# Kernel optimization log

Measured on AMD Instinct MI355X. Metric: run time of the kernel, lower is better.

Reference implementation:

```python
import jax, jax.numpy as jnp
import numpy as np

E, B, D, H, Z = 8, 16384, 512, 512, 64   # experts, batch, input_dim, hidden, latent
NHID = 2                                 # num_mlp_layers - 1 hidden-to-hidden layers


def setup_inputs() -> dict:
    key = jax.random.key(0)
    ks = jax.random.split(key, 12)

    def w(k, shape, fan_in):
        return (jax.random.normal(k, shape, jnp.float32) / np.sqrt(fan_in)).astype(jnp.float32)

    return {
        "x": jax.random.normal(ks[0], (B, D), jnp.float32),
        "eps": jax.random.normal(ks[1], (B, Z), jnp.float32),
        # stacked per-expert parameters (leading axis E)
        "enc_in_w": w(ks[2], (E, D, H), D), "enc_in_b": jnp.zeros((E, H), jnp.float32),
        "enc_hid_w": w(ks[3], (E, NHID, H, H), H), "enc_hid_b": jnp.zeros((E, NHID, H), jnp.float32),
        "mu_w": w(ks[4], (E, H, Z), H), "mu_b": jnp.zeros((E, Z), jnp.float32),
        "lv_w": w(ks[5], (E, H, Z), H), "lv_b": jnp.zeros((E, Z), jnp.float32),
        "dec_in_w": w(ks[6], (E, Z, H), Z), "dec_in_b": jnp.zeros((E, H), jnp.float32),
        "dec_hid_w": w(ks[7], (E, NHID, H, H), H), "dec_hid_b": jnp.zeros((E, NHID, H), jnp.float32),
        "dec_out_w": w(ks[8], (E, H, D), H), "dec_out_b": jnp.zeros((E, D), jnp.float32),
    }


def _moe_forward(x, eps, enc_in_w, enc_in_b, enc_hid_w, enc_hid_b,
                 mu_w, mu_b, lv_w, lv_b,
                 dec_in_w, dec_in_b, dec_hid_w, dec_hid_b, dec_out_w, dec_out_b):
    # ---- every expert tries the problem (dense, all experts over full batch) ----
    h = jax.nn.relu(jnp.einsum('bd,edh->ebh', x, enc_in_w) + enc_in_b[:, None, :])
    for i in range(NHID):
        h = jax.nn.relu(jnp.einsum('ebh,ehk->ebk', h, enc_hid_w[:, i]) + enc_hid_b[:, i, None, :])
    mu = jnp.einsum('ebh,ehz->ebz', h, mu_w) + mu_b[:, None, :]          # [E,B,Z]
    logvar = jnp.einsum('ebh,ehz->ebz', h, lv_w) + lv_b[:, None, :]       # [E,B,Z]
    z = mu + jnp.exp(0.5 * logvar) * eps[None, :, :]                      # reparameterize
    g = jax.nn.relu(jnp.einsum('ebz,ezh->ebh', z, dec_in_w) + dec_in_b[:, None, :])
    for i in range(NHID):
        g = jax.nn.relu(jnp.einsum('ebh,ehk->ebk', g, dec_hid_w[:, i]) + dec_hid_b[:, i, None, :])
    xhat = jnp.einsum('ebh,ehd->ebd', g, dec_out_w) + dec_out_b[:, None, :]  # [E,B,D]

    # ---- per-sample recon loss, pick best expert (torch.min over experts) ----
    recon = jnp.mean((xhat - x[None, :, :]) ** 2, axis=-1)                # [E,B]
    expert_idx = jnp.argmin(recon, axis=0)                                # [B]

    # ---- sparse_others: single fused gather instead of python loop ----
    bi = jnp.arange(x.shape[0])
    return mu[expert_idx, bi], logvar[expert_idx, bi], xhat[expert_idx, bi]


def reference(x, eps, enc_in_w, enc_in_b, enc_hid_w, enc_hid_b,
              mu_w, mu_b, lv_w, lv_b,
              dec_in_w, dec_in_b, dec_hid_w, dec_hid_b, dec_out_w, dec_out_b):
    return _moe_forward(x, eps, enc_in_w, enc_in_b, enc_hid_w, enc_hid_b,
                        mu_w, mu_b, lv_w, lv_b,
                        dec_in_w, dec_in_b, dec_hid_w, dec_hid_b, dec_out_w, dec_out_b)
```

## Files before the change

kernel.cpp:

```cpp
#include <hip/hip_runtime.h>
#include <cstdint>

#define Eexp 8
#define Bb   16384
#define Dd   512
#define Hh   512
#define Zz   64

typedef _Float16 f16x8 __attribute__((ext_vector_type(8)));
typedef _Float16 f16x4 __attribute__((ext_vector_type(4)));
typedef float    f32x4 __attribute__((ext_vector_type(4)));

#define PEREXP     1671168
#define OFF_ENCIN  0
#define OFF_HID0   262144
#define OFF_HID1   524288
#define OFF_MU     786432
#define OFF_LV     819200
#define OFF_DECIN  851968
#define OFF_DHID0  884736
#define OFF_DHID1  1146880
#define OFF_DECOUT 1409024
#define WT_ELEMS   (8 * (size_t)PEREXP)

#define GLL16(g, l) __builtin_amdgcn_global_load_lds( \
    (const __attribute__((address_space(1))) void*)(g), \
    (__attribute__((address_space(3))) void*)(l), 16, 0, 0)

__global__ __launch_bounds__(256)
void tsplit(const float* __restrict__ src, _Float16* __restrict__ dH,
            _Float16* __restrict__ dL, int K, int N, long sStride, long dStride)
{
    __shared__ float t[64][65];
    const int e  = blockIdx.z;
    const int n0 = blockIdx.x * 64, k0 = blockIdx.y * 64;
    const float* S = src + (size_t)e * sStride;
    const int tid = threadIdx.x;
    const int rr = tid >> 4, cc = (tid & 15) * 4;
    #pragma unroll
    for (int p = 0; p < 4; ++p) {
        const float4 v = *reinterpret_cast<const float4*>(
            &S[(size_t)(k0 + rr + p * 16) * N + n0 + cc]);
        t[rr + p * 16][cc + 0] = v.x; t[rr + p * 16][cc + 1] = v.y;
        t[rr + p * 16][cc + 2] = v.z; t[rr + p * 16][cc + 3] = v.w;
    }
    __syncthreads();
    _Float16* DH = dH + (size_t)e * dStride;
    _Float16* DL = dL + (size_t)e * dStride;
    #pragma unroll
    for (int p = 0; p < 4; ++p) {
        const int no = rr + p * 16;
        const float a = t[cc + 0][no], b = t[cc + 1][no];
        const float c = t[cc + 2][no], d = t[cc + 3][no];
        const _Float16 ha = (_Float16)a, hb = (_Float16)b;
        const _Float16 hc = (_Float16)c, hd = (_Float16)d;
        f16x4 hv = {ha, hb, hc, hd};
        f16x4 lv = {(_Float16)(a - (float)ha), (_Float16)(b - (float)hb),
                    (_Float16)(c - (float)hc), (_Float16)(d - (float)hd)};
        *reinterpret_cast<f16x4*>(&DH[(size_t)(n0 + no) * K + k0 + cc]) = hv;
        *reinterpret_cast<f16x4*>(&DL[(size_t)(n0 + no) * K + k0 + cc]) = lv;
    }
}

__global__ __launch_bounds__(256)
void xsplit(const float4* __restrict__ src, f16x4* __restrict__ dh,
            f16x4* __restrict__ dl)
{
    const int i = blockIdx.x * 256 + threadIdx.x;
    const float4 v = src[i];
    const _Float16 h0 = (_Float16)v.x, h1 = (_Float16)v.y;
    const _Float16 h2 = (_Float16)v.z, h3 = (_Float16)v.w;
    f16x4 hv = {h0, h1, h2, h3};
    f16x4 lv = {(_Float16)(v.x - (float)h0), (_Float16)(v.y - (float)h1),
                (_Float16)(v.z - (float)h2), (_Float16)(v.w - (float)h3)};
    dh[i] = hv; dl[i] = lv;
}

template<int BN, int MODE>
__global__ __launch_bounds__(256, 2)
void gemm_sp(const _Float16* __restrict__ Ah, const _Float16* __restrict__ Al,
             const _Float16* __restrict__ Wh0, const _Float16* __restrict__ Wl0,
             const float* __restrict__ bias0,
             float* __restrict__ Cf0, _Float16* __restrict__ Ch0,
             _Float16* __restrict__ Cl0,
             const _Float16* __restrict__ Wh1, const _Float16* __restrict__ Wl1,
             const float* __restrict__ bias1, float* __restrict__ Cf1,
             int Ka, int Nout)
{
    constexpr int BM = 128, BK = 32;
    constexpr int WN = BN / 2;
    constexpr int NF = WN / 16;
    constexpr int CPW = BN / 64;
    __shared__ __align__(16) _Float16 sAh[BM * BK], sAl[BM * BK];
    __shared__ __align__(16) _Float16 sWh[BN * BK], sWl[BN * BK];

    const int nY = (MODE == 2) ? 2 : (Nout / BN);
    int wg = blockIdx.x;
    wg = (wg & 7) * (gridDim.x >> 3) + (wg >> 3);
    const int bx = wg / nY;
    const int by = wg % nY;

    const _Float16* WhP = Wh0; const _Float16* WlP = Wl0;
    const float* biasP = bias0; float* CfP = Cf0;
    if (MODE == 2 && by == 1) { WhP = Wh1; WlP = Wl1; biasP = bias1; CfP = Cf1; }

    const int tid  = threadIdx.x;
    const int lane = tid & 63;
    const int wid  = tid >> 6;
    const int wr = wid >> 1, wc = wid & 1;
    const int row0 = bx * BM;
    const int col0 = (MODE == 2) ? 0 : by * BN;

    f32x4 acc[4][NF];
    #pragma unroll
    for (int i = 0; i < 4; ++i)
        #pragma unroll
        for (int j = 0; j < NF; ++j) acc[i][j] = {0.f, 0.f, 0.f, 0.f};

    for (int k0 = 0; k0 < Ka; k0 += BK) {
        __syncthreads();
        #pragma unroll
        for (int p = 0; p < 2; ++p) {
            const int q  = wid * 2 + p;
            const int rl = q * 16 + (lane >> 2);
            const int c  = (lane & 3) ^ ((rl >> 1) & 3);
            const size_t gi = (size_t)(row0 + rl) * Ka + k0 + c * 8;
            GLL16(Ah + gi, &sAh[q * 512]);
            GLL16(Al + gi, &sAl[q * 512]);
        }
        #pragma unroll
        for (int p = 0; p < CPW; ++p) {
            const int q  = wid * CPW + p;
            const int rl = q * 16 + (lane >> 2);
            const int c  = (lane & 3) ^ ((rl >> 1) & 3);
            const size_t gi = (size_t)(col0 + rl) * Ka + k0 + c * 8;
            GLL16(WhP + gi, &sWh[q * 512]);
            GLL16(WlP + gi, &sWl[q * 512]);
        }
        __syncthreads();
        f16x8 fah[4], fal[4], fwh[NF], fwl[NF];
        #pragma unroll
        for (int mf = 0; mf < 4; ++mf) {
            const int r = wr * 64 + mf * 16 + (lane & 15);
            const int c = (lane >> 4) ^ ((r >> 1) & 3);
            const int idx = r * 32 + c * 8;
            fah[mf] = *reinterpret_cast<f16x8*>(&sAh[idx]);
            fal[mf] = *reinterpret_cast<f16x8*>(&sAl[idx]);
        }
        #pragma unroll
        for (int nf = 0; nf < NF; ++nf) {
            const int r = wc * WN + nf * 16 + (lane & 15);
            const int c = (lane >> 4) ^ ((r >> 1) & 3);
            const int idx = r * 32 + c * 8;
            fwh[nf] = *reinterpret_cast<f16x8*>(&sWh[idx]);
            fwl[nf] = *reinterpret_cast<f16x8*>(&sWl[idx]);
        }
        #pragma unroll
        for (int mf = 0; mf < 4; ++mf)
            #pragma unroll
            for (int nf = 0; nf < NF; ++nf) {
                acc[mf][nf] = __builtin_amdgcn_mfma_f32_16x16x32_f16(
                    fah[mf], fwh[nf], acc[mf][nf], 0, 0, 0);
                acc[mf][nf] = __builtin_amdgcn_mfma_f32_16x16x32_f16(
                    fah[mf], fwl[nf], acc[mf][nf], 0, 0, 0);
                acc[mf][nf] = __builtin_amdgcn_mfma_f32_16x16x32_f16(
                    fal[mf], fwh[nf], acc[mf][nf], 0, 0, 0);
            }
    }

    #pragma unroll
    for (int nf = 0; nf < NF; ++nf) {
        const int col = col0 + wc * WN + nf * 16 + (lane & 15);
        const float bv = biasP[col];
        #pragma unroll
        for (int mf = 0; mf < 4; ++mf)
            #pragma unroll
            for (int j = 0; j < 4; ++j) {
                const int rowg = row0 + wr * 64 + mf * 16 + (lane >> 4) * 4 + j;
                float v = acc[mf][nf][j] + bv;
                if (MODE == 0) {
                    v = fmaxf(v, 0.f);
                    const _Float16 h = (_Float16)v;
                    const _Float16 l = (_Float16)(v - (float)h);
                    Ch0[(size_t)rowg * Nout + col] = h;
                    Cl0[(size_t)rowg * Nout + col] = l;
                } else {
                    CfP[(size_t)rowg * Nout + col] = v;
                }
            }
    }
}

__global__ __launch_bounds__(256)
void z_kernel(const float4* __restrict__ mu, const float4* __restrict__ lv,
              const float4* __restrict__ eps, f16x4* __restrict__ zh,
              f16x4* __restrict__ zl)
{
    const int i = blockIdx.x * 256 + threadIdx.x;
    const float4 m = mu[i], l = lv[i], e = eps[i];
    float4 r;
    r.x = m.x + expf(0.5f * l.x) * e.x;
    r.y = m.y + expf(0.5f * l.y) * e.y;
    r.z = m.z + expf(0.5f * l.z) * e.z;
    r.w = m.w + expf(0.5f * l.w) * e.w;
    const _Float16 h0 = (_Float16)r.x, h1 = (_Float16)r.y;
    const _Float16 h2 = (_Float16)r.z, h3 = (_Float16)r.w;
    f16x4 hv = {h0, h1, h2, h3};
    f16x4 lvv = {(_Float16)(r.x - (float)h0), (_Float16)(r.y - (float)h1),
                 (_Float16)(r.z - (float)h2), (_Float16)(r.w - (float)h3)};
    zh[i] = hv; zl[i] = lvv;
}

__global__ __launch_bounds__(256)
void recon_kernel(const float* __restrict__ xhat, const float* __restrict__ x,
                  float* __restrict__ recon)
{
    const int wave = threadIdx.x >> 6;
    const int lane = threadIdx.x & 63;
    const int row  = blockIdx.x * 4 + wave;
    const float4* xh = reinterpret_cast<const float4*>(&xhat[(size_t)row * Dd]);
    const float4* xx = reinterpret_cast<const float4*>(&x[(size_t)row * Dd]);
    float s = 0.f;
    #pragma unroll
    for (int it = 0; it < 2; ++it) {
        const float4 a = xh[lane + it * 64];
        const float4 b = xx[lane + it * 64];
        float d;
        d = a.x - b.x; s = fmaf(d, d, s);
        d = a.y - b.y; s = fmaf(d, d, s);
        d = a.z - b.z; s = fmaf(d, d, s);
        d = a.w - b.w; s = fmaf(d, d, s);
    }
    #pragma unroll
    for (int off = 32; off > 0; off >>= 1) s += __shfl_down(s, off);
    if (lane == 0) recon[row] = s * (1.0f / 512.0f);
}

__global__ __launch_bounds__(256)
void select_kernel(const float* __restrict__ recon, float* __restrict__ best,
                   const float* __restrict__ mu_e, const float* __restrict__ lv_e,
                   const float* __restrict__ xhat,
                   float* __restrict__ out_mu, float* __restrict__ out_lv,
                   float* __restrict__ out_xh, int isFirst)
{
    const int wave = threadIdx.x >> 6;
    const int lane = threadIdx.x & 63;
    const int row  = blockIdx.x * 4 + wave;
    const float r  = recon[row];
    const bool cond = isFirst || (r < best[row]);
    if (cond) {
        if (lane == 0) best[row] = r;
        out_mu[(size_t)row * Zz + lane] = mu_e[(size_t)row * Zz + lane];
        out_lv[(size_t)row * Zz + lane] = lv_e[(size_t)row * Zz + lane];
        const float4* src = reinterpret_cast<const float4*>(&xhat[(size_t)row * Dd]);
        float4*       dst = reinterpret_cast<float4*>(&out_xh[(size_t)row * Dd]);
        dst[lane]      = src[lane];
        dst[lane + 64] = src[lane + 64];
    }
}

extern "C" void kernel_launch(void* const* d_in, const int* in_sizes, int n_in,
                              void* d_out, int out_size, void* d_ws, size_t ws_size,
                              hipStream_t stream)
{
    const float* x         = (const float*)d_in[0];
    const float* eps       = (const float*)d_in[1];
    const float* enc_in_w  = (const float*)d_in[2];
    const float* enc_in_b  = (const float*)d_in[3];
    const float* enc_hid_w = (const float*)d_in[4];
    const float* enc_hid_b = (const float*)d_in[5];
    const float* mu_w      = (const float*)d_in[6];
    const float* mu_b      = (const float*)d_in[7];
    const float* lv_w      = (const float*)d_in[8];
    const float* lv_b      = (const float*)d_in[9];
    const float* dec_in_w  = (const float*)d_in[10];
    const float* dec_in_b  = (const float*)d_in[11];
    const float* dec_hid_w = (const float*)d_in[12];
    const float* dec_hid_b = (const float*)d_in[13];
    const float* dec_out_w = (const float*)d_in[14];
    const float* dec_out_b = (const float*)d_in[15];

    const size_t BD = (size_t)Bb * 512;
    const size_t BZ = (size_t)Bb * 64;

    _Float16* wtH = (_Float16*)d_ws;
    _Float16* wtL = wtH + WT_ELEMS;
    _Float16* xh  = wtL + WT_ELEMS;
    _Float16* xl  = xh + BD;
    _Float16* aH  = xl + BD;
    _Float16* aL  = aH + BD;
    _Float16* bH  = aL + BD;
    _Float16* bL  = bH + BD;
    _Float16* zh  = bL + BD;
    _Float16* zl  = zh + BZ;
    float* fbase  = (float*)(zl + BZ);
    float* xhat   = fbase;
    float* mu_e   = xhat + BD;
    float* lv_e   = mu_e + BZ;
    float* rec    = lv_e + BZ;
    float* best   = rec + Bb;

    float* out_mu = (float*)d_out;
    float* out_lv = out_mu + (size_t)Bb * Zz;
    float* out_xh = out_lv + (size_t)Bb * Zz;

    const dim3 blk(256);

    tsplit<<<dim3(8, 8, 8), blk, 0, stream>>>(enc_in_w,           wtH + OFF_ENCIN,  wtL + OFF_ENCIN,  512, 512, 262144, PEREXP);
    tsplit<<<dim3(8, 8, 8), blk, 0, stream>>>(enc_hid_w,          wtH + OFF_HID0,   wtL + OFF_HID0,   512, 512, 524288, PEREXP);
    tsplit<<<dim3(8, 8, 8), blk, 0, stream>>>(enc_hid_w + 262144, wtH + OFF_HID1,   wtL + OFF_HID1,   512, 512, 524288, PEREXP);
    tsplit<<<dim3(1, 8, 8), blk, 0, stream>>>(mu_w,               wtH + OFF_MU,     wtL + OFF_MU,     512,  64,  32768, PEREXP);
    tsplit<<<dim3(1, 8, 8), blk, 0, stream>>>(lv_w,               wtH + OFF_LV,     wtL + OFF_LV,     512,  64,  32768, PEREXP);
    tsplit<<<dim3(8, 1, 8), blk, 0, stream>>>(dec_in_w,           wtH + OFF_DECIN,  wtL + OFF_DECIN,   64, 512,  32768, PEREXP);
    tsplit<<<dim3(8, 8, 8), blk, 0, stream>>>(dec_hid_w,          wtH + OFF_DHID0,  wtL + OFF_DHID0,  512, 512, 524288, PEREXP);
    tsplit<<<dim3(8, 8, 8), blk, 0, stream>>>(dec_hid_w + 262144, wtH + OFF_DHID1,  wtL + OFF_DHID1,  512, 512, 524288, PEREXP);
    tsplit<<<dim3(8, 8, 8), blk, 0, stream>>>(dec_out_w,          wtH + OFF_DECOUT, wtL + OFF_DECOUT, 512, 512, 262144, PEREXP);
    xsplit<<<dim3(BD / 4 / 256), blk, 0, stream>>>(
        (const float4*)x, (f16x4*)xh, (f16x4*)xl);

    const dim3 gBig(512);
    const dim3 gDual(256);
    const dim3 gRow(Bb / 4);
    const dim3 gZ(BZ / 4 / 256);

    for (int e = 0; e < Eexp; ++e) {
        const size_t wo = (size_t)e * PEREXP;
        gemm_sp<128, 0><<<gBig, blk, 0, stream>>>(
            xh, xl, wtH + wo + OFF_ENCIN, wtL + wo + OFF_ENCIN,
            enc_in_b + (size_t)e * Hh, nullptr, aH, aL,
            nullptr, nullptr, nullptr, nullptr, Dd, Hh);
        gemm_sp<128, 0><<<gBig, blk, 0, stream>>>(
            aH, aL, wtH + wo + OFF_HID0, wtL + wo + OFF_HID0,
            enc_hid_b + ((size_t)e * 2 + 0) * Hh, nullptr, bH, bL,
            nullptr, nullptr, nullptr, nullptr, Hh, Hh);
        gemm_sp<128, 0><<<gBig, blk, 0, stream>>>(
            bH, bL, wtH + wo + OFF_HID1, wtL + wo + OFF_HID1,
            enc_hid_b + ((size_t)e * 2 + 1) * Hh, nullptr, aH, aL,
            nullptr, nullptr, nullptr, nullptr, Hh, Hh);
        gemm_sp<64, 2><<<gDual, blk, 0, stream>>>(
            aH, aL, wtH + wo + OFF_MU, wtL + wo + OFF_MU,
            mu_b + (size_t)e * Zz, mu_e, nullptr, nullptr,
            wtH + wo + OFF_LV, wtL + wo + OFF_LV,
            lv_b + (size_t)e * Zz, lv_e, Hh, Zz);
        z_kernel<<<gZ, blk, 0, stream>>>(
            (const float4*)mu_e, (const float4*)lv_e, (const float4*)eps,
            (f16x4*)zh, (f16x4*)zl);
        gemm_sp<128, 0><<<gBig, blk, 0, stream>>>(
            zh, zl, wtH + wo + OFF_DECIN, wtL + wo + OFF_DECIN,
            dec_in_b + (size_t)e * Hh, nullptr, bH, bL,
            nullptr, nullptr, nullptr, nullptr, Zz, Hh);
        gemm_sp<128, 0><<<gBig, blk, 0, stream>>>(
            bH, bL, wtH + wo + OFF_DHID0, wtL + wo + OFF_DHID0,
            dec_hid_b + ((size_t)e * 2 + 0) * Hh, nullptr, aH, aL,
            nullptr, nullptr, nullptr, nullptr, Hh, Hh);
        gemm_sp<128, 0><<<gBig, blk, 0, stream>>>(
            aH, aL, wtH + wo + OFF_DHID1, wtL + wo + OFF_DHID1,
            dec_hid_b + ((size_t)e * 2 + 1) * Hh, nullptr, bH, bL,
            nullptr, nullptr, nullptr, nullptr, Hh, Hh);
        gemm_sp<128, 1><<<gBig, blk, 0, stream>>>(
            bH, bL, wtH + wo + OFF_DECOUT, wtL + wo + OFF_DECOUT,
            dec_out_b + (size_t)e * Dd, xhat, nullptr, nullptr,
            nullptr, nullptr, nullptr, nullptr, Hh, Dd);
        recon_kernel<<<gRow, blk, 0, stream>>>(xhat, x, rec);
        select_kernel<<<gRow, blk, 0, stream>>>(
            rec, best, mu_e, lv_e, xhat, out_mu, out_lv, out_xh, e == 0 ? 1 : 0);
    }
}
```

Measured before the change: 2.060 ms.

## Double-buffer split-fp16 GEMM with 512-thread blocks and fuse recon into decoder output

Replaces the single-buffered GEMM with a 512-thread, 128x128-tile kernel that double-buffers the global-to-LDS loads and uses vmcnt waits so the next K-tile's loads overlap the current MFMA work. The hidden-layer epilogue stages packed hi/lo fp16 results through LDS so global stores are coalesced. The output-layer epilogue computes per-row partial squared errors, which removes the separate recon kernel and its re-read of xhat. The mu/logvar head is merged into a single 128-column tile. In exchange, select now sums 16 partial rows, and LDS use per block is higher, which may limit occupancy.

```diff
diff --git a/kernel.cpp b/kernel.cpp
--- a/kernel.cpp
+++ b/kernel.cpp
@@ -76,89 +76,89 @@
     dh[i] = hv; dl[i] = lv;
 }
 
-template<int BN, int MODE>
-__global__ __launch_bounds__(256, 2)
-void gemm_sp(const _Float16* __restrict__ Ah, const _Float16* __restrict__ Al,
-             const _Float16* __restrict__ Wh0, const _Float16* __restrict__ Wl0,
-             const float* __restrict__ bias0,
-             float* __restrict__ Cf0, _Float16* __restrict__ Ch0,
-             _Float16* __restrict__ Cl0,
-             const _Float16* __restrict__ Wh1, const _Float16* __restrict__ Wl1,
-             const float* __restrict__ bias1, float* __restrict__ Cf1,
-             int Ka, int Nout)
-{
-    constexpr int BM = 128, BK = 32;
-    constexpr int WN = BN / 2;
-    constexpr int NF = WN / 16;
-    constexpr int CPW = BN / 64;
-    __shared__ __align__(16) _Float16 sAh[BM * BK], sAl[BM * BK];
-    __shared__ __align__(16) _Float16 sWh[BN * BK], sWl[BN * BK];
-
-    const int nY = (MODE == 2) ? 2 : (Nout / BN);
+template<int MODE>
+__global__ __launch_bounds__(512, 4)
+void gemm5(const _Float16* __restrict__ Ah, const _Float16* __restrict__ Al,
+           const _Float16* __restrict__ Wh, const _Float16* __restrict__ Wl,
+           const float* __restrict__ bias0, const float* __restrict__ bias1,
+           float* __restrict__ Cf, _Float16* __restrict__ Ch,
+           _Float16* __restrict__ Cl, float* __restrict__ Cf1,
+           const float* __restrict__ Xin, float* __restrict__ rec16,
+           int Ka)
+{
+    constexpr int nY = (MODE == 2) ? 1 : 4;
+    __shared__ __align__(16) _Float16 sbuf[2][16384];
+
     int wg = blockIdx.x;
     wg = (wg & 7) * (gridDim.x >> 3) + (wg >> 3);
     const int bx = wg / nY;
     const int by = wg % nY;
 
-    const _Float16* WhP = Wh0; const _Float16* WlP = Wl0;
-    const float* biasP = bias0; float* CfP = Cf0;
-    if (MODE == 2 && by == 1) { WhP = Wh1; WlP = Wl1; biasP = bias1; CfP = Cf1; }
-
     const int tid  = threadIdx.x;
     const int lane = tid & 63;
     const int wid  = tid >> 6;
-    const int wr = wid >> 1, wc = wid & 1;
-    const int row0 = bx * BM;
-    const int col0 = (MODE == 2) ? 0 : by * BN;
-
-    f32x4 acc[4][NF];
+    const int wr = wid >> 2;
+    const int wc = wid & 3;
+    const int row0 = bx * 128;
+    const int col0 = by * 128;
+
+    f32x4 acc[4][2];
     #pragma unroll
     for (int i = 0; i < 4; ++i)
         #pragma unroll
-        for (int j = 0; j < NF; ++j) acc[i][j] = {0.f, 0.f, 0.f, 0.f};
-
-    for (int k0 = 0; k0 < Ka; k0 += BK) {
-        __syncthreads();
-        #pragma unroll
-        for (int p = 0; p < 2; ++p) {
-            const int q  = wid * 2 + p;
-            const int rl = q * 16 + (lane >> 2);
-            const int c  = (lane & 3) ^ ((rl >> 1) & 3);
-            const size_t gi = (size_t)(row0 + rl) * Ka + k0 + c * 8;
-            GLL16(Ah + gi, &sAh[q * 512]);
-            GLL16(Al + gi, &sAl[q * 512]);
-        }
-        #pragma unroll
-        for (int p = 0; p < CPW; ++p) {
-            const int q  = wid * CPW + p;
-            const int rl = q * 16 + (lane >> 2);
-            const int c  = (lane & 3) ^ ((rl >> 1) & 3);
-            const size_t gi = (size_t)(col0 + rl) * Ka + k0 + c * 8;
-            GLL16(WhP + gi, &sWh[q * 512]);
-            GLL16(WlP + gi, &sWl[q * 512]);
-        }
-        __syncthreads();
-        f16x8 fah[4], fal[4], fwh[NF], fwl[NF];
+        for (int j = 0; j < 2; ++j) acc[i][j] = {0.f, 0.f, 0.f, 0.f};
+
+    const int clane = lane >> 2;
+    const int cslot = lane & 3;
+
+    #define STAGE(buf, kk0)                                                   \
+    {                                                                         \
+        _Pragma("unroll")                                                     \
+        for (int p = 0; p < 4; ++p) {                                         \
+            const int q  = wid * 4 + p;                                       \
+            const int ch = q & 7;                                             \
+            const int rl = ch * 16 + clane;                                   \
+            const int cs = cslot ^ ((rl >> 1) & 3);                           \
+            const bool isA = q < 16;                                          \
+            const size_t gi = (size_t)((isA ? row0 : col0) + rl) * Ka         \
+                              + (kk0) + cs * 8;                               \
+            const _Float16* gp = (q < 8) ? (Ah + gi) : (q < 16) ? (Al + gi)   \
+                               : (q < 24) ? (Wh + gi) : (Wl + gi);            \
+            GLL16(gp, &sbuf[buf][q * 512]);                                   \
+        }                                                                     \
+    }
+
+    const int NT = Ka >> 5;
+    STAGE(0, 0)
+    if (NT > 1) STAGE(1, 32)
+
+    for (int t = 0; t < NT; ++t) {
+        if (t + 1 < NT) { asm volatile("s_waitcnt vmcnt(4)" ::: "memory"); }
+        else            { asm volatile("s_waitcnt vmcnt(0)" ::: "memory"); }
+        __builtin_amdgcn_s_barrier();
+        asm volatile("" ::: "memory");
+
+        const _Float16* Sb = sbuf[t & 1];
+        f16x8 fah[4], fal[4], fwh[2], fwl[2];
         #pragma unroll
         for (int mf = 0; mf < 4; ++mf) {
             const int r = wr * 64 + mf * 16 + (lane & 15);
-            const int c = (lane >> 4) ^ ((r >> 1) & 3);
-            const int idx = r * 32 + c * 8;
-            fah[mf] = *reinterpret_cast<f16x8*>(&sAh[idx]);
-            fal[mf] = *reinterpret_cast<f16x8*>(&sAl[idx]);
-        }
-        #pragma unroll
-        for (int nf = 0; nf < NF; ++nf) {
-            const int r = wc * WN + nf * 16 + (lane & 15);
-            const int c = (lane >> 4) ^ ((r >> 1) & 3);
-            const int idx = r * 32 + c * 8;
-            fwh[nf] = *reinterpret_cast<f16x8*>(&sWh[idx]);
-            fwl[nf] = *reinterpret_cast<f16x8*>(&sWl[idx]);
-        }
+            const int u = (lane >> 4) ^ ((r >> 1) & 3);
+            fah[mf] = *reinterpret_cast<const f16x8*>(&Sb[r * 32 + u * 8]);
+            fal[mf] = *reinterpret_cast<const f16x8*>(&Sb[4096 + r * 32 + u * 8]);
+        }
+        #pragma unroll
+        for (int nf = 0; nf < 2; ++nf) {
+            const int r = wc * 32 + nf * 16 + (lane & 15);
+            const int u = (lane >> 4) ^ ((r >> 1) & 3);
+            fwh[nf] = *reinterpret_cast<const f16x8*>(&Sb[8192 + r * 32 + u * 8]);
+            fwl[nf] = *reinterpret_cast<const f16x8*>(&Sb[12288 + r * 32 + u * 8]);
+        }
+        __builtin_amdgcn_s_setprio(1);
         #pragma unroll
         for (int mf = 0; mf < 4; ++mf)
             #pragma unroll
-            for (int nf = 0; nf < NF; ++nf) {
+            for (int nf = 0; nf < 2; ++nf) {
                 acc[mf][nf] = __builtin_amdgcn_mfma_f32_16x16x32_f16(
                     fah[mf], fwh[nf], acc[mf][nf], 0, 0, 0);
                 acc[mf][nf] = __builtin_amdgcn_mfma_f32_16x16x32_f16(
@@ -166,28 +166,105 @@
                 acc[mf][nf] = __builtin_amdgcn_mfma_f32_16x16x32_f16(
                     fal[mf], fwh[nf], acc[mf][nf], 0, 0, 0);
             }
-    }
-
-    #pragma unroll
-    for (int nf = 0; nf < NF; ++nf) {
-        const int col = col0 + wc * WN + nf * 16 + (lane & 15);
-        const float bv = biasP[col];
-        #pragma unroll
-        for (int mf = 0; mf < 4; ++mf)
-            #pragma unroll
-            for (int j = 0; j < 4; ++j) {
-                const int rowg = row0 + wr * 64 + mf * 16 + (lane >> 4) * 4 + j;
-                float v = acc[mf][nf][j] + bv;
-                if (MODE == 0) {
-                    v = fmaxf(v, 0.f);
+        __builtin_amdgcn_s_setprio(0);
+
+        asm volatile("" ::: "memory");
+        __builtin_amdgcn_s_barrier();
+        asm volatile("" ::: "memory");
+        if (t + 2 < NT) STAGE((t & 1), (t + 2) * 32)
+    }
+    #undef STAGE
+
+    if (MODE == 0) {
+        uint32_t* sb32 = reinterpret_cast<uint32_t*>(&sbuf[0][0]);
+        #pragma unroll
+        for (int nf = 0; nf < 2; ++nf) {
+            const int cl = wc * 32 + nf * 16 + (lane & 15);
+            const float bv = bias0[col0 + cl];
+            #pragma unroll
+            for (int mf = 0; mf < 4; ++mf)
+                #pragma unroll
+                for (int j = 0; j < 4; ++j) {
+                    const int rl = wr * 64 + mf * 16 + (lane >> 4) * 4 + j;
+                    float v = fmaxf(acc[mf][nf][j] + bv, 0.f);
                     const _Float16 h = (_Float16)v;
                     const _Float16 l = (_Float16)(v - (float)h);
-                    Ch0[(size_t)rowg * Nout + col] = h;
-                    Cl0[(size_t)rowg * Nout + col] = l;
-                } else {
-                    CfP[(size_t)rowg * Nout + col] = v;
+                    const uint32_t pk = (uint32_t)__builtin_bit_cast(uint16_t, h)
+                                      | ((uint32_t)__builtin_bit_cast(uint16_t, l) << 16);
+                    sb32[rl * 128 + cl] = pk;
+                }
+        }
+        asm volatile("" ::: "memory");
+        __builtin_amdgcn_s_barrier();
+        asm volatile("" ::: "memory");
+        #pragma unroll
+        for (int i = 0; i < 8; ++i) {
+            const int rl = i * 16 + (tid >> 5);
+            const int c4 = (tid & 31) * 4;
+            uint32_t w0 = sb32[rl * 128 + c4 + 0];
+            uint32_t w1 = sb32[rl * 128 + c4 + 1];
+            uint32_t w2 = sb32[rl * 128 + c4 + 2];
+            uint32_t w3 = sb32[rl * 128 + c4 + 3];
+            f16x4 hv = {__builtin_bit_cast(_Float16, (uint16_t)(w0 & 0xffff)),
+                        __builtin_bit_cast(_Float16, (uint16_t)(w1 & 0xffff)),
+                        __builtin_bit_cast(_Float16, (uint16_t)(w2 & 0xffff)),
+                        __builtin_bit_cast(_Float16, (uint16_t)(w3 & 0xffff))};
+            f16x4 lv = {__builtin_bit_cast(_Float16, (uint16_t)(w0 >> 16)),
+                        __builtin_bit_cast(_Float16, (uint16_t)(w1 >> 16)),
+                        __builtin_bit_cast(_Float16, (uint16_t)(w2 >> 16)),
+                        __builtin_bit_cast(_Float16, (uint16_t)(w3 >> 16))};
+            const size_t o = (size_t)(row0 + rl) * 512 + col0 + c4;
+            *reinterpret_cast<f16x4*>(&Ch[o]) = hv;
+            *reinterpret_cast<f16x4*>(&Cl[o]) = lv;
+        }
+    } else if (MODE == 1) {
+        float rsum[4][4];
+        #pragma unroll
+        for (int mf = 0; mf < 4; ++mf)
+            #pragma unroll
+            for (int j = 0; j < 4; ++j) rsum[mf][j] = 0.f;
+        #pragma unroll
+        for (int nf = 0; nf < 2; ++nf) {
+            const int col = col0 + wc * 32 + nf * 16 + (lane & 15);
+            const float bv = bias0[col];
+            #pragma unroll
+            for (int mf = 0; mf < 4; ++mf)
+                #pragma unroll
+                for (int j = 0; j < 4; ++j) {
+                    const int row = row0 + wr * 64 + mf * 16 + (lane >> 4) * 4 + j;
+                    const float v = acc[mf][nf][j] + bv;
+                    Cf[(size_t)row * 512 + col] = v;
+                    const float d = v - Xin[(size_t)row * 512 + col];
+                    rsum[mf][j] += d * d;
+                }
+        }
+        #pragma unroll
+        for (int mf = 0; mf < 4; ++mf)
+            #pragma unroll
+            for (int j = 0; j < 4; ++j) {
+                float s = rsum[mf][j];
+                s += __shfl_xor(s, 1); s += __shfl_xor(s, 2);
+                s += __shfl_xor(s, 4); s += __shfl_xor(s, 8);
+                if ((lane & 15) == 0) {
+                    const int row = row0 + wr * 64 + mf * 16 + (lane >> 4) * 4 + j;
+                    rec16[(size_t)(by * 4 + wc) * Bb + row] = s;
                 }
             }
+    } else {
+        #pragma unroll
+        for (int nf = 0; nf < 2; ++nf) {
+            const int col = wc * 32 + nf * 16 + (lane & 15);
+            const float bv = (col < 64) ? bias0[col] : bias1[col - 64];
+            #pragma unroll
+            for (int mf = 0; mf < 4; ++mf)
+                #pragma unroll
+                for (int j = 0; j < 4; ++j) {
+                    const int row = row0 + wr * 64 + mf * 16 + (lane >> 4) * 4 + j;
+                    const float v = acc[mf][nf][j] + bv;
+                    if (col < 64) Cf [(size_t)row * 64 + col]      = v;
+                    else          Cf1[(size_t)row * 64 + col - 64] = v;
+                }
+        }
     }
 }
 
@@ -212,32 +289,7 @@
 }
 
 __global__ __launch_bounds__(256)
-void recon_kernel(const float* __restrict__ xhat, const float* __restrict__ x,
-                  float* __restrict__ recon)
-{
-    const int wave = threadIdx.x >> 6;
-    const int lane = threadIdx.x & 63;
-    const int row  = blockIdx.x * 4 + wave;
-    const float4* xh = reinterpret_cast<const float4*>(&xhat[(size_t)row * Dd]);
-    const float4* xx = reinterpret_cast<const float4*>(&x[(size_t)row * Dd]);
-    float s = 0.f;
-    #pragma unroll
-    for (int it = 0; it < 2; ++it) {
-        const float4 a = xh[lane + it * 64];
-        const float4 b = xx[lane + it * 64];
-        float d;
-        d = a.x - b.x; s = fmaf(d, d, s);
-        d = a.y - b.y; s = fmaf(d, d, s);
-        d = a.z - b.z; s = fmaf(d, d, s);
-        d = a.w - b.w; s = fmaf(d, d, s);
-    }
-    #pragma unroll
-    for (int off = 32; off > 0; off >>= 1) s += __shfl_down(s, off);
-    if (lane == 0) recon[row] = s * (1.0f / 512.0f);
-}
-
-__global__ __launch_bounds__(256)
-void select_kernel(const float* __restrict__ recon, float* __restrict__ best,
+void select_kernel(const float* __restrict__ rec16, float* __restrict__ best,
                    const float* __restrict__ mu_e, const float* __restrict__ lv_e,
                    const float* __restrict__ xhat,
                    float* __restrict__ out_mu, float* __restrict__ out_lv,
@@ -246,7 +298,10 @@
     const int wave = threadIdx.x >> 6;
     const int lane = threadIdx.x & 63;
     const int row  = blockIdx.x * 4 + wave;
-    const float r  = recon[row];
+    float r = 0.f;
+    #pragma unroll
+    for (int p = 0; p < 16; ++p) r += rec16[(size_t)p * Bb + row];
+    r *= (1.0f / 512.0f);
     const bool cond = isFirst || (r < best[row]);
     if (cond) {
         if (lane == 0) best[row] = r;
@@ -297,8 +352,8 @@
     float* xhat   = fbase;
     float* mu_e   = xhat + BD;
     float* lv_e   = mu_e + BZ;
-    float* rec    = lv_e + BZ;
-    float* best   = rec + Bb;
+    float* rec16  = lv_e + BZ;
+    float* best   = rec16 + (size_t)16 * Bb;
 
     float* out_mu = (float*)d_out;
     float* out_lv = out_mu + (size_t)Bb * Zz;
@@ -318,51 +373,50 @@
     xsplit<<<dim3(BD / 4 / 256), blk, 0, stream>>>(
         (const float4*)x, (f16x4*)xh, (f16x4*)xl);
 
+    const dim3 gblk(512);
     const dim3 gBig(512);
-    const dim3 gDual(256);
+    const dim3 gHead(128);
     const dim3 gRow(Bb / 4);
     const dim3 gZ(BZ / 4 / 256);
 
     for (int e = 0; e < Eexp; ++e) {
         const size_t wo = (size_t)e * PEREXP;
-        gemm_sp<128, 0><<<gBig, blk, 0, stream>>>(
+        gemm5<0><<<gBig, gblk, 0, stream>>>(
             xh, xl, wtH + wo + OFF_ENCIN, wtL + wo + OFF_ENCIN,
-            enc_in_b + (size_t)e * Hh, nullptr, aH, aL,
-            nullptr, nullptr, nullptr, nullptr, Dd, Hh);
-        gemm_sp<128, 0><<<gBig, blk, 0, stream>>>(
+            enc_in_b + (size_t)e * Hh, nullptr,
+            nullptr, aH, aL, nullptr, nullptr, nullptr, Dd);
+        gemm5<0><<<gBig, gblk, 0, stream>>>(
             aH, aL, wtH + wo + OFF_HID0, wtL + wo + OFF_HID0,
-            enc_hid_b + ((size_t)e * 2 + 0) * Hh, nullptr, bH, bL,
-            nullptr, nullptr, nullptr, nullptr, Hh, Hh);
-        gemm_sp<128, 0><<<gBig, blk, 0, stream>>>(
+            enc_hid_b + ((size_t)e * 2 + 0) * Hh, nullptr,
+            nullptr, bH, bL, nullptr, nullptr, nullptr, Hh);
+        gemm5<0><<<gBig, gblk, 0, stream>>>(
             bH, bL, wtH + wo + OFF_HID1, wtL + wo + OFF_HID1,
-            enc_hid_b + ((size_t)e * 2 + 1) * Hh, nullptr, aH, aL,
-            nullptr, nullptr, nullptr, nullptr, Hh, Hh);
-        gemm_sp<64, 2><<<gDual, blk, 0, stream>>>(
+            enc_hid_b + ((size_t)e * 2 + 1) * Hh, nullptr,
+            nullptr, aH, aL, nullptr, nullptr, nullptr, Hh);
+        gemm5<2><<<gHead, gblk, 0, stream>>>(
             aH, aL, wtH + wo + OFF_MU, wtL + wo + OFF_MU,
-            mu_b + (size_t)e * Zz, mu_e, nullptr, nullptr,
-            wtH + wo + OFF_LV, wtL + wo + OFF_LV,
-            lv_b + (size_t)e * Zz, lv_e, Hh, Zz);
+            mu_b + (size_t)e * Zz, lv_b + (size_t)e * Zz,
+            mu_e, nullptr, nullptr, lv_e, nullptr, nullptr, Hh);
         z_kernel<<<gZ, blk, 0, stream>>>(
             (const float4*)mu_e, (const float4*)lv_e, (const float4*)eps,
             (f16x4*)zh, (f16x4*)zl);
-        gemm_sp<128, 0><<<gBig, blk, 0, stream>>>(
+        gemm5<0><<<gBig, gblk, 0, stream>>>(
             zh, zl, wtH + wo + OFF_DECIN, wtL + wo + OFF_DECIN,
-            dec_in_b + (size_t)e * Hh, nullptr, bH, bL,
-            nullptr, nullptr, nullptr, nullptr, Zz, Hh);
-        gemm_sp<128, 0><<<gBig, blk, 0, stream>>>(
+            dec_in_b + (size_t)e * Hh, nullptr,
+            nullptr, bH, bL, nullptr, nullptr, nullptr, Zz);
+        gemm5<0><<<gBig, gblk, 0, stream>>>(
             bH, bL, wtH + wo + OFF_DHID0, wtL + wo + OFF_DHID0,
-            dec_hid_b + ((size_t)e * 2 + 0) * Hh, nullptr, aH, aL,
-            nullptr, nullptr, nullptr, nullptr, Hh, Hh);
-        gemm_sp<128, 0><<<gBig, blk, 0, stream>>>(
+            dec_hid_b + ((size_t)e * 2 + 0) * Hh, nullptr,
+            nullptr, aH, aL, nullptr, nullptr, nullptr, Hh);
+        gemm5<0><<<gBig, gblk, 0, stream>>>(
             aH, aL, wtH + wo + OFF_DHID1, wtL + wo + OFF_DHID1,
-            dec_hid_b + ((size_t)e * 2 + 1) * Hh, nullptr, bH, bL,
-            nullptr, nullptr, nullptr, nullptr, Hh, Hh);
-        gemm_sp<128, 1><<<gBig, blk, 0, stream>>>(
+            dec_hid_b + ((size_t)e * 2 + 1) * Hh, nullptr,
+            nullptr, bH, bL, nullptr, nullptr, nullptr, Hh);
+        gemm5<1><<<gBig, gblk, 0, stream>>>(
             bH, bL, wtH + wo + OFF_DECOUT, wtL + wo + OFF_DECOUT,
-            dec_out_b + (size_t)e * Dd, xhat, nullptr, nullptr,
-            nullptr, nullptr, nullptr, nullptr, Hh, Dd);
-        recon_kernel<<<gRow, blk, 0, stream>>>(xhat, x, rec);
+            dec_out_b + (size_t)e * Dd, nullptr,
+            xhat, nullptr, nullptr, nullptr, x, rec16, Hh);
         select_kernel<<<gRow, blk, 0, stream>>>(
-            rec, best, mu_e, lv_e, xhat, out_mu, out_lv, out_xh, e == 0 ? 1 : 0);
-    }
-}
+            rec16, best, mu_e, lv_e, xhat, out_mu, out_lv, out_xh, e == 0 ? 1 : 0);
+    }
+}
```

Result: faster. 1.889 ms (-8.3%).
